# Kernel tuning notes

Hardware: AMD Instinct MI355X
Metric: run time of the kernel (lower is better)

## Reference

```python
import jax, jax.numpy as jnp
import numpy as np

H = 128   # hidden dim (all hidden_* params)
B = 256   # number of compound graphs in batch
NG = 4000  # number of compound groups (masked-out comp nodes)
NA = 10000  # number of anchors

LRELU = lambda x: jax.nn.leaky_relu(x, 0.1)
seg_sum = jax.ops.segment_sum


def seg_softmax(s, seg, n):
    # scatter_softmax over segments keyed by destination node
    m = jax.ops.segment_max(s, seg, num_segments=n)
    e = jnp.exp(s - m[seg])
    d = seg_sum(e, seg, num_segments=n)
    return e / d[seg]


def gru_cell(x, h, Wih, Whh, bih, bhh):
    # torch.nn.GRUCell semantics
    gi = x @ Wih.T + bih
    gh = h @ Whh.T + bhh
    ir, iz, inn = jnp.split(gi, 3, axis=-1)
    hr, hz, hn = jnp.split(gh, 3, axis=-1)
    r = jax.nn.sigmoid(ir + hr)
    z = jax.nn.sigmoid(iz + hz)
    n = jnp.tanh(inn + r * hn)
    return (1.0 - z) * n + z * h


def conv_stack(x, src, dst, Ws, bs, Wout, bout, n):
    # AtomConv/AnchorConv stack with dense-concat skip and output projection
    feats = [x]
    h = x
    for W, b in zip(Ws, bs):
        h = LRELU(seg_sum(h[src], dst, num_segments=n) @ W + b)
        feats.append(h)
    return LRELU(jnp.concatenate(feats, -1) @ Wout + bout)


def _forward(vert_x, site_x, masf_x, prot_edge_attr, prom_edge_attr,
             W_emb, b_emb,
             gwm_W_main, gwm_W_s2m, gwm_W_gate_main, gwm_b_gate_main,
             gwm_W_q, gwm_W_k, gwm_W_merge, gwm_W_gate_super, gwm_b_gate_super,
             gru_m_Wih, gru_m_Whh, gru_m_bih, gru_m_bhh,
             gru_s_Wih, gru_s_Whh, gru_s_bih, gru_s_bhh,
             W_site0, b_site0, W_site1, b_site1, W_site_out, b_site_out,
             W_masf0, b_masf0, W_masf1, b_masf1, W_masf_out, b_masf_out,
             W_anch0, b_anch0, W_anch1, b_anch1, W_anch_out, b_anch_out,
             W_dsite, b_dsite, W_dcomp, b_dcomp,
             vert_src, vert_dst, vert_batch, comp_src, comp_dst,
             site_src, site_dst, masf_src, masf_dst,
             prot_src, prot_dst, prom_src, prom_dst, anch_src, anch_dst,
             idx_ag_a, idx_ag_g, idx_aa_0, idx_aa_1, idx_gg_0, idx_gg_1):
    Nv = vert_x.shape[0]
    Ns = site_x.shape[0]
    Nm = masf_x.shape[0]
    # --- GraphConv_module: vertex embedding + super-node init ---
    vert = LRELU(vert_x @ W_emb + b_emb)
    supe = seg_sum(vert, vert_batch, num_segments=B)
    inv_sqrt_h = np.float32(1.0 / np.sqrt(H))
    # --- GWM iterations (shared GRU_main / GRU_super) ---
    for t in range(gwm_W_main.shape[0]):
        agg = seg_sum(vert[vert_src], vert_dst, num_segments=Nv)  # neighbor sum
        h_main = LRELU(agg @ gwm_W_main[t])
        trans = LRELU(supe @ gwm_W_s2m[t])[vert_batch]  # super -> main
        z = jax.nn.sigmoid(jnp.concatenate([h_main, trans], -1) @ gwm_W_gate_main[t] + gwm_b_gate_main[t])
        vert = gru_cell(z * h_main + (1.0 - z) * trans, vert,
                        gru_m_Wih, gru_m_Whh, gru_m_bih, gru_m_bhh)
        # main -> super attention (k_head = 1)
        q = (supe @ gwm_W_q[t])[vert_batch]
        k = vert @ gwm_W_k[t]
        score = jnp.sum(q * k, -1, keepdims=True) * inv_sqrt_h  # [Nv,1]
        attn = seg_softmax(score, vert_batch, B)
        pooled = seg_sum(attn * vert, vert_batch, num_segments=B)
        m_sup = LRELU(pooled @ gwm_W_merge[t])
        zs = jax.nn.sigmoid(jnp.concatenate([m_sup, supe], -1) @ gwm_W_gate_super[t] + gwm_b_gate_super[t])
        supe = gru_cell(zs * m_sup + (1.0 - zs) * supe, supe,
                        gru_s_Wih, gru_s_Whh, gru_s_bih, gru_s_bhh)
    # --- Group_module: uniform edge softmax (softmax of ones == 1/deg) ---
    w_g = seg_softmax(jnp.zeros((comp_src.shape[0], 1), vert.dtype), comp_dst, NG)
    group = seg_sum(w_g * vert[comp_src], comp_dst, num_segments=NG)  # [NG,H]
    # --- AtomConv_module / MasfConv_module ---
    site_out = conv_stack(site_x, site_src, site_dst, [W_site0, W_site1],
                          [b_site0, b_site1], W_site_out, b_site_out, Ns)
    masf_out = conv_stack(masf_x, masf_src, masf_dst, [W_masf0, W_masf1],
                          [b_masf0, b_masf1], W_masf_out, b_masf_out, Nm)
    # --- Anchor_module (UpwardConv with scatter_softmax(6 - dist) weights) ---
    # fill_anchor_graph's padded scatter + gather is fused into direct indexing
    w_p = seg_softmax(6.0 - prot_edge_attr, prot_dst, NA)
    anchor_atom = seg_sum(w_p * site_out[prot_src], prot_dst, num_segments=NA)
    w_m = seg_softmax(6.0 - prom_edge_attr, prom_dst, NA)
    anchor_masf = seg_sum(w_m * masf_out[prom_src], prom_dst, num_segments=NA)
    # --- AnchorAnchor_module (Affsrc == 'all': concat atom/masif anchor feats) ---
    anch = jnp.concatenate([anchor_atom, anchor_masf], -1)  # [NA,2H]
    anch_out = conv_stack(anch, anch_src, anch_dst, [W_anch0, W_anch1],
                          [b_anch0, b_anch1], W_anch_out, b_anch_out, NA)
    # --- Distance_pred_module ---
    pa = LRELU(anch_out @ W_dsite + b_dsite)
    pg = LRELU(group @ W_dcomp + b_dcomp)
    eps = np.float32(1e-6)  # torch.pairwise_distance eps
    pd = lambda a, b: jnp.sqrt(jnp.sum((a - b + eps) ** 2, -1, keepdims=True))
    ag = pd(pa[idx_ag_a], pg[idx_ag_g])
    aa = pd(pa[idx_aa_0], pa[idx_aa_1])
    gg = pd(pg[idx_gg_0], pg[idx_gg_1])
    return jnp.concatenate([ag, aa, gg], 0)  # [Pag+Paa+Pgg, 1]


def setup_inputs():
    key = jax.random.key(0)
    ks = iter(jax.random.split(key, 100))
    f32 = jnp.float32

    def nrm(shape, s=0.05):
        return jax.random.normal(next(ks), shape, f32) * s

    def ri(n, hi):
        return jax.random.randint(next(ks), (n,), 0, hi, dtype=jnp.int32)

    def zeros(*shape):
        return jnp.zeros(shape, f32)

    Nv, Ev, Ec = 20000, 80000, 40000
    Ns, Es = 80000, 320000
    Nm, Em = 80000, 320000
    Ep, Ea = 160000, 80000
    Pag, Paa, Pgg = 200000, 100000, 50000
    FV, Fs, Fm, D = 82, 256, 320, 2
    inp = {}
    inp["vert_x"] = nrm((Nv, FV), 1.0)
    inp["site_x"] = nrm((Ns, Fs), 1.0)
    inp["masf_x"] = nrm((Nm, Fm), 1.0)
    inp["prot_edge_attr"] = jax.random.uniform(next(ks), (Ep, 1), f32) * 6.0
    inp["prom_edge_attr"] = jax.random.uniform(next(ks), (Ep, 1), f32) * 6.0
    inp["vert_src"] = ri(Ev, Nv); inp["vert_dst"] = ri(Ev, Nv)
    inp["vert_batch"] = jnp.sort(ri(Nv, B))
    inp["comp_src"] = ri(Ec, Nv); inp["comp_dst"] = ri(Ec, NG)
    inp["site_src"] = ri(Es, Ns); inp["site_dst"] = ri(Es, Ns)
    inp["masf_src"] = ri(Em, Nm); inp["masf_dst"] = ri(Em, Nm)
    inp["prot_src"] = ri(Ep, Ns); inp["prot_dst"] = ri(Ep, NA)
    inp["prom_src"] = ri(Ep, Nm); inp["prom_dst"] = ri(Ep, NA)
    inp["anch_src"] = ri(Ea, NA); inp["anch_dst"] = ri(Ea, NA)
    inp["idx_ag_a"] = ri(Pag, NA); inp["idx_ag_g"] = ri(Pag, NG)
    inp["idx_aa_0"] = ri(Paa, NA); inp["idx_aa_1"] = ri(Paa, NA)
    inp["idx_gg_0"] = ri(Pgg, NG); inp["idx_gg_1"] = ri(Pgg, NG)
    inp["W_emb"] = nrm((FV, H)); inp["b_emb"] = zeros(H)
    inp["gwm_W_main"] = nrm((D, H, H)); inp["gwm_W_s2m"] = nrm((D, H, H))
    inp["gwm_W_gate_main"] = nrm((D, 2 * H, H)); inp["gwm_b_gate_main"] = zeros(D, H)
    inp["gwm_W_q"] = nrm((D, H, H)); inp["gwm_W_k"] = nrm((D, H, H))
    inp["gwm_W_merge"] = nrm((D, H, H))
    inp["gwm_W_gate_super"] = nrm((D, 2 * H, H)); inp["gwm_b_gate_super"] = zeros(D, H)
    for p in ["m", "s"]:
        inp["gru_%s_Wih" % p] = nrm((3 * H, H)); inp["gru_%s_Whh" % p] = nrm((3 * H, H))
        inp["gru_%s_bih" % p] = zeros(3 * H); inp["gru_%s_bhh" % p] = zeros(3 * H)
    inp["W_site0"] = nrm((Fs, H)); inp["b_site0"] = zeros(H)
    inp["W_site1"] = nrm((H, H)); inp["b_site1"] = zeros(H)
    inp["W_site_out"] = nrm((Fs + 2 * H, H)); inp["b_site_out"] = zeros(H)
    inp["W_masf0"] = nrm((Fm, H)); inp["b_masf0"] = zeros(H)
    inp["W_masf1"] = nrm((H, H)); inp["b_masf1"] = zeros(H)
    inp["W_masf_out"] = nrm((Fm + 2 * H, H)); inp["b_masf_out"] = zeros(H)
    inp["W_anch0"] = nrm((2 * H, H)); inp["b_anch0"] = zeros(H)
    inp["W_anch1"] = nrm((H, H)); inp["b_anch1"] = zeros(H)
    inp["W_anch_out"] = nrm((4 * H, H)); inp["b_anch_out"] = zeros(H)
    inp["W_dsite"] = nrm((H, H)); inp["b_dsite"] = zeros(H)
    inp["W_dcomp"] = nrm((H, H)); inp["b_dcomp"] = zeros(H)
    return inp


def reference(vert_x, site_x, masf_x, prot_edge_attr, prom_edge_attr,
              W_emb, b_emb,
              gwm_W_main, gwm_W_s2m, gwm_W_gate_main, gwm_b_gate_main,
              gwm_W_q, gwm_W_k, gwm_W_merge, gwm_W_gate_super, gwm_b_gate_super,
              gru_m_Wih, gru_m_Whh, gru_m_bih, gru_m_bhh,
              gru_s_Wih, gru_s_Whh, gru_s_bih, gru_s_bhh,
              W_site0, b_site0, W_site1, b_site1, W_site_out, b_site_out,
              W_masf0, b_masf0, W_masf1, b_masf1, W_masf_out, b_masf_out,
              W_anch0, b_anch0, W_anch1, b_anch1, W_anch_out, b_anch_out,
              W_dsite, b_dsite, W_dcomp, b_dcomp,
              vert_src, vert_dst, vert_batch, comp_src, comp_dst,
              site_src, site_dst, masf_src, masf_dst,
              prot_src, prot_dst, prom_src, prom_dst, anch_src, anch_dst,
              idx_ag_a, idx_ag_g, idx_aa_0, idx_aa_1, idx_gg_0, idx_gg_1):
    return _forward(vert_x, site_x, masf_x, prot_edge_attr, prom_edge_attr,
                    W_emb, b_emb,
                    gwm_W_main, gwm_W_s2m, gwm_W_gate_main, gwm_b_gate_main,
                    gwm_W_q, gwm_W_k, gwm_W_merge, gwm_W_gate_super, gwm_b_gate_super,
                    gru_m_Wih, gru_m_Whh, gru_m_bih, gru_m_bhh,
                    gru_s_Wih, gru_s_Whh, gru_s_bih, gru_s_bhh,
                    W_site0, b_site0, W_site1, b_site1, W_site_out, b_site_out,
                    W_masf0, b_masf0, W_masf1, b_masf1, W_masf_out, b_masf_out,
                    W_anch0, b_anch0, W_anch1, b_anch1, W_anch_out, b_anch_out,
                    W_dsite, b_dsite, W_dcomp, b_dcomp,
                    vert_src, vert_dst, vert_batch, comp_src, comp_dst,
                    site_src, site_dst, masf_src, masf_dst,
                    prot_src, prot_dst, prom_src, prom_dst, anch_src, anch_dst,
                    idx_ag_a, idx_ag_g, idx_aa_0, idx_aa_1, idx_gg_0, idx_gg_1)
```

## Files before the change

### kernel.cpp

```cpp
#include <hip/hip_runtime.h>
#include <math.h>

#define HD 128

typedef __bf16 bf16x8 __attribute__((ext_vector_type(8)));
typedef unsigned short u16x8 __attribute__((ext_vector_type(8)));
typedef float f32x4 __attribute__((ext_vector_type(4)));

__device__ __forceinline__ unsigned short f2bf(float f) {
    unsigned u = __float_as_uint(f);
    unsigned r = u + 0x7FFFu + ((u >> 16) & 1u);
    return (unsigned short)(r >> 16);
}

#define MAXW 32
struct WDesc { const float* src; unsigned short* dst; int K, N, Kpad, tr; };
struct WBatch { WDesc d[MAXW]; };

__global__ void convert_weights(WBatch wb)
{
    WDesc d = wb.d[blockIdx.y];
    long total = (long)d.N * d.Kpad;
    long i = (long)blockIdx.x * 256 + threadIdx.x;
    if (i >= total) return;
    int n = (int)(i / d.Kpad), k = (int)(i % d.Kpad);
    float v = 0.f;
    if (k < d.K) v = d.tr ? d.src[(size_t)k * d.N + n] : d.src[(size_t)n * d.K + k];
    d.dst[i] = f2bf(v);
}

__global__ __launch_bounds__(256)
void gemm_mfma(const float* __restrict__ A0, const float* __restrict__ A1,
               const float* __restrict__ A2, int K0, int K1, int K2,
               int lda0, int lda1, int lda2,
               const unsigned short* __restrict__ WT, int Kpad,
               const float* __restrict__ bias, float* __restrict__ C,
               int M, int N, int act,
               const float* __restrict__ G1, const float* __restrict__ G2)
{
    __shared__ __align__(16) unsigned short sA[2][64][40];
    __shared__ __align__(16) unsigned short sW[2][128][40];

    const int tid = threadIdx.x;
    const int lane = tid & 63, w = tid >> 6;
    const int mBase = blockIdx.x * 64;
    const int nBase = blockIdx.y * 128;
    const int Ktot = K0 + K1 + K2;
    const int colb = w * 32;
    const int c16 = lane & 15, g = lane >> 4;

    f32x4 acc[4][2];
#pragma unroll
    for (int i = 0; i < 4; ++i)
#pragma unroll
        for (int j = 0; j < 2; ++j) acc[i][j] = (f32x4){0.f, 0.f, 0.f, 0.f};

    const int kTiles = (Ktot + 31) / 32;

    auto loadTile = [&](int kt, float f[8], u16x8& h0, u16x8& h1) {
        const int k0g = kt * 32;
        const float* Ab; int lda, kloc, segK;
        if (k0g < K0)           { Ab = A0; lda = lda0; kloc = k0g;           segK = K0; }
        else if (k0g < K0 + K1) { Ab = A1; lda = lda1; kloc = k0g - K0;      segK = K1; }
        else                    { Ab = A2; lda = lda2; kloc = k0g - K0 - K1; segK = K2; }
        int row = tid >> 2, kq = (tid & 3) * 8;
        int gr = mBase + row;
        if (gr < M && ((lda & 3) == 0) && (kloc + kq + 8 <= segK)) {
            const float* ap = Ab + (size_t)gr * lda + kloc + kq;
            float4 v0 = *(const float4*)ap, v1 = *(const float4*)(ap + 4);
            f[0] = v0.x; f[1] = v0.y; f[2] = v0.z; f[3] = v0.w;
            f[4] = v1.x; f[5] = v1.y; f[6] = v1.z; f[7] = v1.w;
        } else {
#pragma unroll
            for (int i = 0; i < 8; ++i) {
                int kk = kloc + kq + i;
                f[i] = (gr < M && kk < segK) ? Ab[(size_t)gr * lda + kk] : 0.f;
            }
        }
        int col = tid >> 1, kh = (tid & 1) * 16;
        const unsigned short* wp = WT + (size_t)(nBase + col) * Kpad + k0g + kh;
        h0 = *(const u16x8*)wp;
        h1 = *(const u16x8*)(wp + 8);
    };
    auto stageWrite = [&](int buf, const float f[8], u16x8 h0, u16x8 h1) {
        int row = tid >> 2, kq = (tid & 3) * 8;
        u16x8 h;
#pragma unroll
        for (int i = 0; i < 8; ++i) h[i] = f2bf(f[i]);
        *(u16x8*)&sA[buf][row][kq] = h;
        int col = tid >> 1, kh = (tid & 1) * 16;
        *(u16x8*)&sW[buf][col][kh] = h0;
        *(u16x8*)&sW[buf][col][kh + 8] = h1;
    };
    auto compute = [&](int buf) {
        bf16x8 bfr0 = __builtin_bit_cast(bf16x8, *(const u16x8*)&sW[buf][colb + c16][g * 8]);
        bf16x8 bfr1 = __builtin_bit_cast(bf16x8, *(const u16x8*)&sW[buf][colb + 16 + c16][g * 8]);
#pragma unroll
        for (int rf = 0; rf < 4; ++rf) {
            bf16x8 af = __builtin_bit_cast(bf16x8, *(const u16x8*)&sA[buf][rf * 16 + c16][g * 8]);
            acc[rf][0] = __builtin_amdgcn_mfma_f32_16x16x32_bf16(af, bfr0, acc[rf][0], 0, 0, 0);
            acc[rf][1] = __builtin_amdgcn_mfma_f32_16x16x32_bf16(af, bfr1, acc[rf][1], 0, 0, 0);
        }
    };

    float fN[8]; u16x8 hN0, hN1;
    {
        float fC[8]; u16x8 hC0, hC1;
        loadTile(0, fC, hC0, hC1);
        stageWrite(0, fC, hC0, hC1);
        if (kTiles > 1) loadTile(1, fN, hN0, hN1);
    }
    asm volatile("s_waitcnt lgkmcnt(0)" ::: "memory");
    __builtin_amdgcn_s_barrier();

    int cur = 0;
#pragma unroll 2
    for (int kt = 0; kt < kTiles; ++kt) {
        float fP[8]; u16x8 hP0, hP1;
        const bool pf = (kt + 2 < kTiles);
        if (pf) loadTile(kt + 2, fP, hP0, hP1);
        compute(cur);
        if (kt + 1 < kTiles) stageWrite(cur ^ 1, fN, hN0, hN1);
        asm volatile("s_waitcnt lgkmcnt(0)" ::: "memory");
        __builtin_amdgcn_s_barrier();
        if (pf) {
#pragma unroll
            for (int i = 0; i < 8; ++i) fN[i] = fP[i];
            hN0 = hP0; hN1 = hP1;
        }
        cur ^= 1;
    }

#pragma unroll
    for (int cf = 0; cf < 2; ++cf) {
        int col = nBase + colb + cf * 16 + c16;
        float bb = bias ? bias[col] : 0.f;
#pragma unroll
        for (int rf = 0; rf < 4; ++rf) {
            int r0 = mBase + rf * 16 + g * 4;
#pragma unroll
            for (int r = 0; r < 4; ++r) {
                int gr = r0 + r;
                if (gr >= M) continue;
                size_t o = (size_t)gr * N + col;
                float v = acc[rf][cf][r] + bb;
                if (act == 1) v = v > 0.f ? v : 0.1f * v;
                else if (act == 2) v = 1.f / (1.f + expf(-v));
                else if (act == 3) {
                    float z = 1.f / (1.f + expf(-v));
                    v = z * G1[o] + (1.f - z) * G2[o];
                }
                C[o] = v;
            }
        }
    }
}

__global__ void hist_k(int* __restrict__ cnt, const int* __restrict__ dst, int E)
{
    int i = blockIdx.x * 256 + threadIdx.x;
    if (i < E) atomicAdd(&cnt[dst[i]], 1);
}

#define SCB 4096

__global__ __launch_bounds__(256)
void scan_sums(const int* __restrict__ cnt, int n, int* __restrict__ bsum)
{
    __shared__ int red[256];
    int t = threadIdx.x;
    int base = blockIdx.x * SCB + t * 16;
    int s = 0;
#pragma unroll
    for (int i = 0; i < 16; ++i) { int idx = base + i; if (idx < n) s += cnt[idx]; }
    red[t] = s; __syncthreads();
    for (int st = 128; st > 0; st >>= 1) {
        if (t < st) red[t] += red[t + st];
        __syncthreads();
    }
    if (t == 0) bsum[blockIdx.x] = red[0];
}

__global__ void scan_bsum(int* __restrict__ bsum, int nb)
{
    if (threadIdx.x == 0) {
// ... 8 lines not shown
{
    __shared__ int a0[256], a1[256];
    int t = threadIdx.x;
    int base = blockIdx.x * SCB + t * 16;
    int v[16]; int s = 0;
#pragma unroll
    for (int i = 0; i < 16; ++i) { int idx = base + i; v[i] = (idx < n) ? cnt[idx] : 0; s += v[i]; }
    a0[t] = s; __syncthreads();
    int* cur = a0; int* nxt = a1;
    for (int st = 1; st < 256; st <<= 1) {
        int val = cur[t] + ((t >= st) ? cur[t - st] : 0);
        nxt[t] = val; __syncthreads();
        int* tmp = cur; cur = nxt; nxt = tmp;
    }
    int run = bsum[blockIdx.x] + (t > 0 ? cur[t - 1] : 0);
#pragma unroll
    for (int i = 0; i < 16; ++i) {
        int idx = base + i;
        if (idx < n) {
            rp[idx] = run; run += v[i];
            if (idx == n - 1) rp[n] = run;
        }
    }
}

__global__ void fill_k(int* __restrict__ eidx, int* __restrict__ cursor,
                       const int* __restrict__ dst, int E)
{
    int i = blockIdx.x * 256 + threadIdx.x;
    if (i < E) eidx[atomicAdd(&cursor[dst[i]], 1)] = i;
}

__global__ __launch_bounds__(256)
void seg_gather(float* __restrict__ out, const float* __restrict__ X,
                const int* __restrict__ rowptr, const int* __restrict__ eidx,
                const int* __restrict__ src, const float* __restrict__ wattr,
                const float* __restrict__ bias, int n, int ostride, int ooff,
                int act, int mode)
{
    int d = blockIdx.x * 4 + (threadIdx.x >> 6);
    if (d >= n) return;
    int lane = threadIdx.x & 63;
    int lo = rowptr[d], hi = rowptr[d + 1];
    float w0 = 1.f, mx = 0.f, iden = 0.f;
    if (mode == 2) w0 = (hi > lo) ? 1.f / (float)(hi - lo) : 0.f;
    if (mode == 3) {
        float mxl = -1e30f;
        for (int base = lo; base < hi; base += 64) {
            int i = base + lane;
            if (i < hi) mxl = fmaxf(mxl, 6.f - wattr[eidx[i]]);
        }
#pragma unroll
        for (int o = 32; o; o >>= 1) mxl = fmaxf(mxl, __shfl_xor(mxl, o));
        mx = mxl;
        float dl = 0.f;
        for (int base = lo; base < hi; base += 64) {
            int i = base + lane;
            if (i < hi) dl += expf(6.f - wattr[eidx[i]] - mx);
        }
#pragma unroll
        for (int o = 32; o; o >>= 1) dl += __shfl_xor(dl, o);
        iden = 1.f / dl;
    }

    float ax = 0.f, ay = 0.f;
    int i = lo;
    for (; i + 4 <= hi; i += 4) {
        int e0 = eidx[i], e1 = eidx[i + 1], e2 = eidx[i + 2], e3 = eidx[i + 3];
        int s0 = src ? src[e0] : e0, s1 = src ? src[e1] : e1;
        int s2 = src ? src[e2] : e2, s3 = src ? src[e3] : e3;
        float w0v, w1v, w2v, w3v;
        if (mode == 0) { w0v = w1v = w2v = w3v = 1.f; }
        else if (mode == 1) { w0v = wattr[e0]; w1v = wattr[e1]; w2v = wattr[e2]; w3v = wattr[e3]; }
        else if (mode == 2) { w0v = w1v = w2v = w3v = w0; }
        else {
            w0v = expf(6.f - wattr[e0] - mx) * iden;
            w1v = expf(6.f - wattr[e1] - mx) * iden;
            w2v = expf(6.f - wattr[e2] - mx) * iden;
            w3v = expf(6.f - wattr[e3] - mx) * iden;
        }
        float2 v0 = *(const float2*)(X + (size_t)s0 * HD + 2 * lane);
        float2 v1 = *(const float2*)(X + (size_t)s1 * HD + 2 * lane);
        float2 v2 = *(const float2*)(X + (size_t)s2 * HD + 2 * lane);
        float2 v3 = *(const float2*)(X + (size_t)s3 * HD + 2 * lane);
        ax += w0v * v0.x + w1v * v1.x + w2v * v2.x + w3v * v3.x;
        ay += w0v * v0.y + w1v * v1.y + w2v * v2.y + w3v * v3.y;
    }
    for (; i < hi; ++i) {
        int e = eidx[i];
        int s = src ? src[e] : e;
        float w;
        if (mode == 0) w = 1.f;
        else if (mode == 1) w = wattr[e];
        else if (mode == 2) w = w0;
        else w = expf(6.f - wattr[e] - mx) * iden;
        float2 v = *(const float2*)(X + (size_t)s * HD + 2 * lane);
        ax += w * v.x; ay += w * v.y;
    }
    if (bias) { float2 b = *(const float2*)(bias + 2 * lane); ax += b.x; ay += b.y; }
    if (act == 1) { ax = ax > 0.f ? ax : 0.1f * ax; ay = ay > 0.f ? ay : 0.1f * ay; }
    *(float2*)(out + (size_t)d * ostride + ooff + 2 * lane) = make_float2(ax, ay);
}

__global__ __launch_bounds__(256)
void seg_softmax_csr(float* __restrict__ sc, const int* __restrict__ rowptr,
                     const int* __restrict__ eidx, int n)
{
    int d = blockIdx.x * 4 + (threadIdx.x >> 6);
    if (d >= n) return;
    int lane = threadIdx.x & 63;
    int lo = rowptr[d], hi = rowptr[d + 1];
    float mxl = -1e30f;
    for (int i = lo + lane; i < hi; i += 64) mxl = fmaxf(mxl, sc[eidx[i]]);
#pragma unroll
    for (int o = 32; o; o >>= 1) mxl = fmaxf(mxl, __shfl_xor(mxl, o));
    float dl = 0.f;
    for (int i = lo + lane; i < hi; i += 64) dl += expf(sc[eidx[i]] - mxl);
#pragma unroll
    for (int o = 32; o; o >>= 1) dl += __shfl_xor(dl, o);
    float iden = 1.f / dl;
    for (int i = lo + lane; i < hi; i += 64) {
        int v = eidx[i];
        sc[v] = expf(sc[v] - mxl) * iden;
    }
}

__global__ void gather128(float* __restrict__ out, const float* __restrict__ in,
                          const int* __restrict__ idx, int n)
{
    long i = (long)blockIdx.x * 256 + threadIdx.x;
    if (i >= (long)n * HD) return;
    int r = (int)(i >> 7), f = (int)(i & 127);
    out[i] = in[(size_t)idx[r] * HD + f];
}
// ... 22 lines not shown
#pragma unroll
    for (int i = 0; i < 32; ++i) {
        float4 x = a[i], y = q[i];
        acc += x.x * y.x + x.y * y.y + x.z * y.z + x.w * y.w;
    }
    sc[v] = acc * 0.08838834764831843f;
}

__global__ void pdist_k(float* __restrict__ out, const float* __restrict__ A,
                        const float* __restrict__ Bm, const int* __restrict__ ia,
                        const int* __restrict__ ib, int P)
{
    int p = blockIdx.x * 256 + threadIdx.x;
    if (p >= P) return;
    const float4* a = (const float4*)(A + (size_t)ia[p] * HD);
    const float4* b = (const float4*)(Bm + (size_t)ib[p] * HD);
    float acc = 0.f;
#pragma unroll
    for (int i = 0; i < 32; ++i) {
        float4 x = a[i], y = b[i];
        float d0 = x.x - y.x + 1e-6f, d1 = x.y - y.y + 1e-6f;
        float d2 = x.z - y.z + 1e-6f, d3 = x.w - y.w + 1e-6f;
        acc += d0 * d0 + d1 * d1 + d2 * d2 + d3 * d3;
    }
    out[p] = sqrtf(acc);
}


static inline unsigned gupd(size_t n) { return (unsigned)((n + 255) / 256); }
static inline unsigned gup4(size_t n) { return (unsigned)((n + 3) / 4); }

struct WArena { unsigned short* p; int Kpad; };

static void gemm3s(hipStream_t st, const float* A0, int K0, const float* A1, int K1,
                   const float* A2, int K2, WArena wa, const float* bias,
                   float* C, int M, int N, int act,
                   const float* G1 = nullptr, const float* G2 = nullptr)
{
    dim3 g((M + 63) / 64, N / 128);
    hipLaunchKernelGGL(gemm_mfma, g, dim3(256), 0, st, A0, A1, A2, K0, K1, K2,
                       K0, K1, K2, wa.p, wa.Kpad, bias, C, M, N, act, G1, G2);
}
static void gemm1(hipStream_t st, const float* A, int K, WArena wa, const float* bias,
                  float* C, int M, int N, int act)
{ gemm3s(st, A, K, nullptr, 0, nullptr, 0, wa, bias, C, M, N, act); }
static void gemm2g(hipStream_t st, const float* A0, int K0, const float* A1, int K1,
                   WArena wa, const float* bias, float* C, int M, int N, int act,
                   const float* G1 = nullptr, const float* G2 = nullptr)
{ gemm3s(st, A0, K0, A1, K1, nullptr, 0, wa, bias, C, M, N, act, G1, G2); }

extern "C" void kernel_launch(void* const* d_in, const int* in_sizes, int n_in,
                              void* d_out, int out_size, void* d_ws, size_t ws_size,
                              hipStream_t stream)
{
    (void)n_in; (void)out_size;
    const float* vert_x  = (const float*)d_in[0];
    const float* site_x  = (const float*)d_in[1];
    const float* masf_x  = (const float*)d_in[2];
    const float* prot_ea = (const float*)d_in[3];
    const float* prom_ea = (const float*)d_in[4];
    const int* vert_src = (const int*)d_in[5];
    const int* vert_dst = (const int*)d_in[6];
    const int* vbatch   = (const int*)d_in[7];
    const int* comp_src = (const int*)d_in[8];
    const int* comp_dst = (const int*)d_in[9];
    const int* site_src = (const int*)d_in[10];
    const int* site_dst = (const int*)d_in[11];
    const int* masf_src = (const int*)d_in[12];
    const int* masf_dst = (const int*)d_in[13];
    const int* prot_src = (const int*)d_in[14];
    const int* prot_dst = (const int*)d_in[15];
    const int* prom_src = (const int*)d_in[16];
    const int* prom_dst = (const int*)d_in[17];
    const int* anch_src = (const int*)d_in[18];
    const int* anch_dst = (const int*)d_in[19];
    const int* ag_a = (const int*)d_in[20];
    const int* ag_g = (const int*)d_in[21];
    const int* aa0  = (const int*)d_in[22];
    const int* aa1  = (const int*)d_in[23];
    const int* gg0  = (const int*)d_in[24];
    const int* gg1  = (const int*)d_in[25];
    const float* W_emb = (const float*)d_in[26];
// ... 30 lines not shown
    const float* W_a0 = (const float*)d_in[57];
    const float* b_a0 = (const float*)d_in[58];
    const float* W_a1 = (const float*)d_in[59];
    const float* b_a1 = (const float*)d_in[60];
    const float* W_ao = (const float*)d_in[61];
    const float* b_ao = (const float*)d_in[62];
    const float* W_ds = (const float*)d_in[63];
    const float* b_ds = (const float*)d_in[64];
    const float* W_dc = (const float*)d_in[65];
    const float* b_dc = (const float*)d_in[66];

    const int B = 256, NG = 4000, NA = 10000, Ns = 80000, Nm = 80000;
    const int Nv = in_sizes[7];
    const int FV = in_sizes[0] / Nv;
    const int Fs = in_sizes[1] / Ns;
    const int Fm = in_sizes[2] / Nm;
    const int Ev = in_sizes[5], Ec = in_sizes[8], Es = in_sizes[10], Em = in_sizes[12];
    const int Ep = in_sizes[14], Ea = in_sizes[18];
    const int Pag = in_sizes[20], Paa = in_sizes[22], Pgg = in_sizes[24];
    const int D = in_sizes[28] / (HD * HD);

    float* ws = (float*)d_ws;
    size_t off = 0;
    auto take = [&](size_t n) { size_t o = off; off += n; return o; };
    float* vert  = ws + take((size_t)Nv * HD);
    float* supe  = ws + take((size_t)B * HD);
    float* qsup  = ws + take((size_t)B * HD);
    float* pool  = ws + take((size_t)B * HD);
    float* msup  = ws + take((size_t)B * HD);
    float* zsup  = ws + take((size_t)B * HD);
    float* gis   = ws + take((size_t)B * 3 * HD);
    float* ghs   = ws + take((size_t)B * 3 * HD);
    float* tsml  = ws + take((size_t)B * HD);
    float* grp   = ws + take((size_t)NG * HD);
    float* site_o = ws + take((size_t)Ns * HD);
    float* masf_o = ws + take((size_t)Nm * HD);
    float* anch  = ws + take((size_t)NA * 2 * HD);
    float* ah1   = ws + take((size_t)NA * HD);
    float* ah2   = ws + take((size_t)NA * HD);
    float* axw   = ws + take((size_t)NA * HD);
    float* aout  = ws + take((size_t)NA * HD);
    float* pa    = ws + take((size_t)NA * HD);
    float* pg    = ws + take((size_t)NG * HD);
    float* score = ws + take((size_t)Nv);
    const size_t NvH = (size_t)Nv * HD, NsH = (size_t)Ns * HD;
    float* T = ws + take(3 * NsH);

    const int nN[8] = {Nv, NG, Ns, Nm, NA, NA, NA, B};
    const int nE[8] = {Ev, Ec, Es, Em, Ep, Ep, Ea, Nv};
    const int* dsts[8] = {vert_dst, comp_dst, site_dst, masf_dst,
                          prot_dst, prom_dst, anch_dst, vbatch};
    int baseN[9], baseE[9];
    baseN[0] = 0; baseE[0] = 0;
    for (int g = 0; g < 8; ++g) { baseN[g + 1] = baseN[g] + nN[g]; baseE[g + 1] = baseE[g] + nE[g]; }
    const int totN = baseN[8], totE = baseE[8];

    int* ib = (int*)(ws + off);
    size_t ioff = 0;
    auto taki = [&](size_t n) { size_t o = ioff; ioff += n; return o; };
    int* cnt_all = ib + taki((size_t)totN);
    int* rp_all  = ib + taki((size_t)totN + 1);
    int* cur_all = ib + taki((size_t)totN);
    int* ei_all  = ib + taki((size_t)totE);
    int* bsum    = ib + taki((size_t)((totN + SCB - 1) / SCB) + 1);
    ioff = (ioff + 7) & ~(size_t)7;

    unsigned short* warena = (unsigned short*)(ib + ioff);
    size_t woff = 0;
    WBatch wb; int nW = 0; long maxWTot = 0;
    auto reg = [&](const float* src, int K, int N, int tr) {
        int Kpad = (K + 31) & ~31;
        unsigned short* dst = warena + woff;
        woff += (size_t)N * Kpad;
        long tot = (long)N * Kpad; if (tot > maxWTot) maxWTot = tot;
// ... 28 lines not shown
    WArena wa_ao = reg(W_ao, 4 * HD, HD, 1);
    WArena wa_ds = reg(W_ds, HD, HD, 1);
    WArena wa_dc = reg(W_dc, HD, HD, 1);

    if (ws_size < off * sizeof(float) + ioff * sizeof(int) + woff * sizeof(unsigned short))
        return;

    {
        dim3 g((unsigned)((maxWTot + 255) / 256), nW);
        hipLaunchKernelGGL(convert_weights, g, dim3(256), 0, stream, wb);
    }

    hipMemsetAsync(cnt_all, 0, (size_t)totN * sizeof(int), stream);
    for (int g = 0; g < 8; ++g)
        hist_k<<<gupd((size_t)nE[g]), 256, 0, stream>>>(cnt_all + baseN[g], dsts[g], nE[g]);
    const int nScanBlocks = (totN + SCB - 1) / SCB;
    scan_sums<<<nScanBlocks, 256, 0, stream>>>(cnt_all, totN, bsum);
    scan_bsum<<<1, 64, 0, stream>>>(bsum, nScanBlocks);
    scan_write<<<nScanBlocks, 256, 0, stream>>>(cnt_all, totN, bsum, rp_all);
    hipMemcpyAsync(cur_all, rp_all, (size_t)totN * sizeof(int), hipMemcpyDeviceToDevice, stream);
    for (int g = 0; g < 8; ++g)
        fill_k<<<gupd((size_t)nE[g]), 256, 0, stream>>>(ei_all, cur_all + baseN[g], dsts[g], nE[g]);

    const int* rp_v = rp_all + baseN[0];
    const int* rp_c = rp_all + baseN[1];
    const int* rp_s = rp_all + baseN[2];
    const int* rp_m = rp_all + baseN[3];
    const int* rp_p = rp_all + baseN[4];
    const int* rp_q = rp_all + baseN[5];
    const int* rp_a = rp_all + baseN[6];
    const int* rp_b = rp_all + baseN[7];
    const int* ei = ei_all;

    gemm1(stream, vert_x, FV, wa_emb, b_emb, vert, Nv, HD, 1);
    seg_gather<<<gup4(B), 256, 0, stream>>>(supe, vert, rp_b, ei, nullptr, nullptr,
                                            nullptr, B, HD, 0, 0, 0);

    float* Ta = T;            float* Tb = T + NvH;     float* Tc = T + 2 * NvH;
    float* Td = T + 3 * NvH;  float* Te = T + 4 * NvH; float* Tf = T + 7 * NvH;
    for (int t = 0; t < D; ++t) {
        const float* bgm = gb_gm + (size_t)t * HD;
        const float* bgs = gb_gs + (size_t)t * HD;

        gemm1(stream, vert, HD, wa_main[t], nullptr, Ta, Nv, HD, 0);
        seg_gather<<<gup4((size_t)Nv), 256, 0, stream>>>(Tb, Ta, rp_v, ei, vert_src,
                                                         nullptr, nullptr, Nv, HD, 0, 1, 0);
        gemm1(stream, supe, HD, wa_s2m[t], nullptr, tsml, B, HD, 1);
        gather128<<<gupd(NvH), 256, 0, stream>>>(Tc, tsml, vbatch, Nv);
        gemm2g(stream, Tb, HD, Tc, HD, wa_gm[t], bgm, Td, Nv, HD, 3, Tb, Tc);
        gemm1(stream, Td, HD, wa_mih, gm_bih, Te, Nv, 3 * HD, 0);
        gemm1(stream, vert, HD, wa_mhh, gm_bhh, Tf, Nv, 3 * HD, 0);
        gru_gate<<<gupd(NvH), 256, 0, stream>>>(vert, Te, Tf, Nv);
        gemm1(stream, vert, HD, wa_k[t], nullptr, Ta, Nv, HD, 0);
        gemm1(stream, supe, HD, wa_q[t], nullptr, qsup, B, HD, 0);
        dot_score<<<gupd((size_t)Nv), 256, 0, stream>>>(score, Ta, qsup, vbatch, Nv);
        seg_softmax_csr<<<gup4(B), 256, 0, stream>>>(score, rp_b, ei, B);
        seg_gather<<<gup4(B), 256, 0, stream>>>(pool, vert, rp_b, ei, nullptr, score,
                                                nullptr, B, HD, 0, 0, 1);
        gemm1(stream, pool, HD, wa_mrg[t], nullptr, msup, B, HD, 1);
        gemm2g(stream, msup, HD, supe, HD, wa_gs[t], bgs, zsup, B, HD, 3, msup, supe);
        gemm1(stream, zsup, HD, wa_sih, gs_bih, gis, B, 3 * HD, 0);
        gemm1(stream, supe, HD, wa_shh, gs_bhh, ghs, B, 3 * HD, 0);
        gru_gate<<<gupd((size_t)B * HD), 256, 0, stream>>>(supe, gis, ghs, B);
    }

    seg_gather<<<gup4((size_t)NG), 256, 0, stream>>>(grp, vert, rp_c, ei, comp_src,
                                                     nullptr, nullptr, NG, HD, 0, 0, 2);

    float* T1 = T; float* T2 = T + NsH; float* T3 = T + 2 * NsH;
    gemm1(stream, site_x, Fs, wa_s0, nullptr, T1, Ns, HD, 0);
    seg_gather<<<gup4((size_t)Ns), 256, 0, stream>>>(T2, T1, rp_s, ei, site_src,
                                                     nullptr, b_s0, Ns, HD, 0, 1, 0);
    gemm1(stream, T2, HD, wa_s1, nullptr, T1, Ns, HD, 0);
    seg_gather<<<gup4((size_t)Ns), 256, 0, stream>>>(T3, T1, rp_s, ei, site_src,
                                                     nullptr, b_s1, Ns, HD, 0, 1, 0);
    gemm3s(stream, site_x, Fs, T2, HD, T3, HD, wa_so, b_so, site_o, Ns, HD, 1);

    gemm1(stream, masf_x, Fm, wa_m0, nullptr, T1, Nm, HD, 0);
    seg_gather<<<gup4((size_t)Nm), 256, 0, stream>>>(T2, T1, rp_m, ei, masf_src,
                                                     nullptr, b_m0, Nm, HD, 0, 1, 0);
    gemm1(stream, T2, HD, wa_m1, nullptr, T1, Nm, HD, 0);
    seg_gather<<<gup4((size_t)Nm), 256, 0, stream>>>(T3, T1, rp_m, ei, masf_src,
                                                     nullptr, b_m1, Nm, HD, 0, 1, 0);
    gemm3s(stream, masf_x, Fm, T2, HD, T3, HD, wa_mo, b_mo, masf_o, Nm, HD, 1);

    seg_gather<<<gup4((size_t)NA), 256, 0, stream>>>(anch, site_o, rp_p, ei, prot_src,
                                                     prot_ea, nullptr, NA, 2 * HD, 0, 0, 3);
    seg_gather<<<gup4((size_t)NA), 256, 0, stream>>>(anch, masf_o, rp_q, ei, prom_src,
                                                     prom_ea, nullptr, NA, 2 * HD, HD, 0, 3);

    gemm1(stream, anch, 2 * HD, wa_a0, nullptr, axw, NA, HD, 0);
    seg_gather<<<gup4((size_t)NA), 256, 0, stream>>>(ah1, axw, rp_a, ei, anch_src,
                                                     nullptr, b_a0, NA, HD, 0, 1, 0);
    gemm1(stream, ah1, HD, wa_a1, nullptr, axw, NA, HD, 0);
    seg_gather<<<gup4((size_t)NA), 256, 0, stream>>>(ah2, axw, rp_a, ei, anch_src,
                                                     nullptr, b_a1, NA, HD, 0, 1, 0);
    gemm3s(stream, anch, 2 * HD, ah1, HD, ah2, HD, wa_ao, b_ao, aout, NA, HD, 1);

    gemm1(stream, aout, HD, wa_ds, b_ds, pa, NA, HD, 1);
    gemm1(stream, grp, HD, wa_dc, b_dc, pg, NG, HD, 1);
    float* outp = (float*)d_out;
    pdist_k<<<gupd((size_t)Pag), 256, 0, stream>>>(outp, pa, pg, ag_a, ag_g, Pag);
    pdist_k<<<gupd((size_t)Paa), 256, 0, stream>>>(outp + Pag, pa, pa, aa0, aa1, Paa);
    pdist_k<<<gupd((size_t)Pgg), 256, 0, stream>>>(outp + Pag + Paa, pg, pg, gg0, gg1, Pgg);
}
```

Measured before the change: 1.330 ms.

## Store site/masf/anchor intermediates in bf16 to halve gather and GEMM traffic

Adds bf16 input and output modes to the MFMA GEMM and the segment-gather kernel, then keeps the site, masf, anchor and compound-group intermediate activations in bf16 instead of fp32. This roughly halves the bytes moved by the irregular gathers and the GEMM A-operand loads, and skips the fp32-to-bf16 conversion that was already done inside the GEMM. In exchange, accumulated values are rounded to bf16 between layers, which adds numerical error, and every call carries per-call dtype flags and extra branches.

New measurement: 1.411 ms. 6.1% more time.

```diff
diff --git a/kernel.cpp b/kernel.cpp
--- a/kernel.cpp
+++ b/kernel.cpp
@@ -11,6 +11,15 @@
     unsigned u = __float_as_uint(f);
     unsigned r = u + 0x7FFFu + ((u >> 16) & 1u);
     return (unsigned short)(r >> 16);
+}
+
+__device__ __forceinline__ float2 ldrow2(const void* X, size_t off, int xbf) {
+    if (xbf) {
+        unsigned u = *(const unsigned*)((const unsigned short*)X + off);
+        return make_float2(__uint_as_float((u & 0xffffu) << 16),
+                           __uint_as_float((u >> 16) << 16));
+    }
+    return *(const float2*)((const float*)X + off);
 }
 
 #define MAXW 32
@@ -30,12 +39,12 @@
 }
 
 __global__ __launch_bounds__(256)
-void gemm_mfma(const float* __restrict__ A0, const float* __restrict__ A1,
-               const float* __restrict__ A2, int K0, int K1, int K2,
-               int lda0, int lda1, int lda2,
+void gemm_mfma(const void* __restrict__ A0, const void* __restrict__ A1,
+               const void* __restrict__ A2, int K0, int K1, int K2,
+               int lda0, int lda1, int lda2, int dt0, int dt1, int dt2,
                const unsigned short* __restrict__ WT, int Kpad,
-               const float* __restrict__ bias, float* __restrict__ C,
-               int M, int N, int act,
+               const float* __restrict__ bias, void* __restrict__ Cv,
+               int M, int N, int act, int obf,
                const float* __restrict__ G1, const float* __restrict__ G2)
 {
     __shared__ __align__(16) unsigned short sA[2][64][40];
@@ -57,24 +66,34 @@
 
     const int kTiles = (Ktot + 31) / 32;
 
-    auto loadTile = [&](int kt, float f[8], u16x8& h0, u16x8& h1) {
+    auto loadTile = [&](int kt, float f[8], u16x8& ha, int& isbf, u16x8& h0, u16x8& h1) {
         const int k0g = kt * 32;
-        const float* Ab; int lda, kloc, segK;
-        if (k0g < K0)           { Ab = A0; lda = lda0; kloc = k0g;           segK = K0; }
-        else if (k0g < K0 + K1) { Ab = A1; lda = lda1; kloc = k0g - K0;      segK = K1; }
-        else                    { Ab = A2; lda = lda2; kloc = k0g - K0 - K1; segK = K2; }
+        const void* Ab; int lda, kloc, segK;
+        if (k0g < K0)           { Ab = A0; lda = lda0; kloc = k0g;           segK = K0; isbf = dt0; }
+        else if (k0g < K0 + K1) { Ab = A1; lda = lda1; kloc = k0g - K0;      segK = K1; isbf = dt1; }
+        else                    { Ab = A2; lda = lda2; kloc = k0g - K0 - K1; segK = K2; isbf = dt2; }
         int row = tid >> 2, kq = (tid & 3) * 8;
         int gr = mBase + row;
-        if (gr < M && ((lda & 3) == 0) && (kloc + kq + 8 <= segK)) {
-            const float* ap = Ab + (size_t)gr * lda + kloc + kq;
-            float4 v0 = *(const float4*)ap, v1 = *(const float4*)(ap + 4);
-            f[0] = v0.x; f[1] = v0.y; f[2] = v0.z; f[3] = v0.w;
-            f[4] = v1.x; f[5] = v1.y; f[6] = v1.z; f[7] = v1.w;
+        if (isbf) {
+            u16x8 z;
+#pragma unroll
+            for (int i = 0; i < 8; ++i) z[i] = 0;
+            ha = (gr < M && kloc + kq + 8 <= segK)
+                 ? *(const u16x8*)((const unsigned short*)Ab + (size_t)gr * lda + kloc + kq)
+                 : z;
         } else {
-#pragma unroll
-            for (int i = 0; i < 8; ++i) {
-                int kk = kloc + kq + i;
-                f[i] = (gr < M && kk < segK) ? Ab[(size_t)gr * lda + kk] : 0.f;
+            const float* Af = (const float*)Ab;
+            if (gr < M && ((lda & 3) == 0) && (kloc + kq + 8 <= segK)) {
+                const float* ap = Af + (size_t)gr * lda + kloc + kq;
+                float4 v0 = *(const float4*)ap, v1 = *(const float4*)(ap + 4);
+                f[0] = v0.x; f[1] = v0.y; f[2] = v0.z; f[3] = v0.w;
+                f[4] = v1.x; f[5] = v1.y; f[6] = v1.z; f[7] = v1.w;
+            } else {
+#pragma unroll
+                for (int i = 0; i < 8; ++i) {
+                    int kk = kloc + kq + i;
+                    f[i] = (gr < M && kk < segK) ? Af[(size_t)gr * lda + kk] : 0.f;
+                }
             }
         }
         int col = tid >> 1, kh = (tid & 1) * 16;
@@ -82,11 +101,14 @@
         h0 = *(const u16x8*)wp;
         h1 = *(const u16x8*)(wp + 8);
     };
-    auto stageWrite = [&](int buf, const float f[8], u16x8 h0, u16x8 h1) {
+    auto stageWrite = [&](int buf, int isbf, const float f[8], u16x8 ha, u16x8 h0, u16x8 h1) {
         int row = tid >> 2, kq = (tid & 3) * 8;
         u16x8 h;
-#pragma unroll
-        for (int i = 0; i < 8; ++i) h[i] = f2bf(f[i]);
+        if (isbf) h = ha;
+        else {
+#pragma unroll
+            for (int i = 0; i < 8; ++i) h[i] = f2bf(f[i]);
+        }
         *(u16x8*)&sA[buf][row][kq] = h;
         int col = tid >> 1, kh = (tid & 1) * 16;
         *(u16x8*)&sW[buf][col][kh] = h0;
@@ -103,12 +125,12 @@
         }
     };
 
-    float fN[8]; u16x8 hN0, hN1;
+    float fN[8]; u16x8 haN, hN0, hN1; int bfN = 0;
     {
-        float fC[8]; u16x8 hC0, hC1;
-        loadTile(0, fC, hC0, hC1);
-        stageWrite(0, fC, hC0, hC1);
-        if (kTiles > 1) loadTile(1, fN, hN0, hN1);
+        float fC[8]; u16x8 haC, hC0, hC1; int bfC;
+        loadTile(0, fC, haC, bfC, hC0, hC1);
+        stageWrite(0, bfC, fC, haC, hC0, hC1);
+        if (kTiles > 1) loadTile(1, fN, haN, bfN, hN0, hN1);
     }
     asm volatile("s_waitcnt lgkmcnt(0)" ::: "memory");
     __builtin_amdgcn_s_barrier();
@@ -116,17 +138,17 @@
     int cur = 0;
 #pragma unroll 2
     for (int kt = 0; kt < kTiles; ++kt) {
-        float fP[8]; u16x8 hP0, hP1;
+        float fP[8]; u16x8 haP, hP0, hP1; int bfP = 0;
         const bool pf = (kt + 2 < kTiles);
-        if (pf) loadTile(kt + 2, fP, hP0, hP1);
+        if (pf) loadTile(kt + 2, fP, haP, bfP, hP0, hP1);
         compute(cur);
-        if (kt + 1 < kTiles) stageWrite(cur ^ 1, fN, hN0, hN1);
+        if (kt + 1 < kTiles) stageWrite(cur ^ 1, bfN, fN, haN, hN0, hN1);
         asm volatile("s_waitcnt lgkmcnt(0)" ::: "memory");
         __builtin_amdgcn_s_barrier();
         if (pf) {
 #pragma unroll
             for (int i = 0; i < 8; ++i) fN[i] = fP[i];
-            hN0 = hP0; hN1 = hP1;
+            haN = haP; hN0 = hP0; hN1 = hP1; bfN = bfP;
         }
         cur ^= 1;
     }
@@ -150,7 +172,8 @@
                     float z = 1.f / (1.f + expf(-v));
                     v = z * G1[o] + (1.f - z) * G2[o];
                 }
-                C[o] = v;
+                if (obf) ((unsigned short*)Cv)[o] = f2bf(v);
+                else     ((float*)Cv)[o] = v;
             }
         }
     }
@@ -225,11 +248,11 @@
 }
 
 __global__ __launch_bounds__(256)
-void seg_gather(float* __restrict__ out, const float* __restrict__ X,
+void seg_gather(void* __restrict__ out, const void* __restrict__ X,
                 const int* __restrict__ rowptr, const int* __restrict__ eidx,
                 const int* __restrict__ src, const float* __restrict__ wattr,
                 const float* __restrict__ bias, int n, int ostride, int ooff,
-                int act, int mode)
+                int act, int mode, int xbf, int obf)
 {
     int d = blockIdx.x * 4 + (threadIdx.x >> 6);
     if (d >= n) return;
@@ -272,10 +295,10 @@
             w2v = expf(6.f - wattr[e2] - mx) * iden;
             w3v = expf(6.f - wattr[e3] - mx) * iden;
         }
-        float2 v0 = *(const float2*)(X + (size_t)s0 * HD + 2 * lane);
-        float2 v1 = *(const float2*)(X + (size_t)s1 * HD + 2 * lane);
-        float2 v2 = *(const float2*)(X + (size_t)s2 * HD + 2 * lane);
-        float2 v3 = *(const float2*)(X + (size_t)s3 * HD + 2 * lane);
+        float2 v0 = ldrow2(X, (size_t)s0 * HD + 2 * lane, xbf);
+        float2 v1 = ldrow2(X, (size_t)s1 * HD + 2 * lane, xbf);
+        float2 v2 = ldrow2(X, (size_t)s2 * HD + 2 * lane, xbf);
+        float2 v3 = ldrow2(X, (size_t)s3 * HD + 2 * lane, xbf);
         ax += w0v * v0.x + w1v * v1.x + w2v * v2.x + w3v * v3.x;
         ay += w0v * v0.y + w1v * v1.y + w2v * v2.y + w3v * v3.y;
     }
@@ -287,12 +310,18 @@
         else if (mode == 1) w = wattr[e];
         else if (mode == 2) w = w0;
         else w = expf(6.f - wattr[e] - mx) * iden;
-        float2 v = *(const float2*)(X + (size_t)s * HD + 2 * lane);
+        float2 v = ldrow2(X, (size_t)s * HD + 2 * lane, xbf);
         ax += w * v.x; ay += w * v.y;
     }
     if (bias) { float2 b = *(const float2*)(bias + 2 * lane); ax += b.x; ay += b.y; }
     if (act == 1) { ax = ax > 0.f ? ax : 0.1f * ax; ay = ay > 0.f ? ay : 0.1f * ay; }
-    *(float2*)(out + (size_t)d * ostride + ooff + 2 * lane) = make_float2(ax, ay);
+    size_t o = (size_t)d * ostride + ooff + 2 * lane;
+    if (obf) {
+        unsigned u = (unsigned)f2bf(ax) | ((unsigned)f2bf(ay) << 16);
+        *(unsigned*)((unsigned short*)out + o) = u;
+    } else {
+        *(float2*)((float*)out + o) = make_float2(ax, ay);
+    }
 }
 
 __global__ __launch_bounds__(256)
@@ -381,22 +410,21 @@
 
 struct WArena { unsigned short* p; int Kpad; };
 
-static void gemm3s(hipStream_t st, const float* A0, int K0, const float* A1, int K1,
-                   const float* A2, int K2, WArena wa, const float* bias,
-                   float* C, int M, int N, int act,
-                   const float* G1 = nullptr, const float* G2 = nullptr)
+static void gemmX(hipStream_t st, const void* A0, int K0, int dt0,
+                  const void* A1, int K1, int dt1,
+                  const void* A2, int K2, int dt2,
+                  WArena wa, const float* bias, void* C, int M, int N,
+                  int act, int obf,
+                  const float* G1 = nullptr, const float* G2 = nullptr)
 {
     dim3 g((M + 63) / 64, N / 128);
     hipLaunchKernelGGL(gemm_mfma, g, dim3(256), 0, st, A0, A1, A2, K0, K1, K2,
-                       K0, K1, K2, wa.p, wa.Kpad, bias, C, M, N, act, G1, G2);
-}
-static void gemm1(hipStream_t st, const float* A, int K, WArena wa, const float* bias,
-                  float* C, int M, int N, int act)
-{ gemm3s(st, A, K, nullptr, 0, nullptr, 0, wa, bias, C, M, N, act); }
-static void gemm2g(hipStream_t st, const float* A0, int K0, const float* A1, int K1,
-                   WArena wa, const float* bias, float* C, int M, int N, int act,
-                   const float* G1 = nullptr, const float* G2 = nullptr)
-{ gemm3s(st, A0, K0, A1, K1, nullptr, 0, wa, bias, C, M, N, act, G1, G2); }
+                       K0, K1, K2, dt0, dt1, dt2, wa.p, wa.Kpad, bias, C, M, N,
+                       act, obf, G1, G2);
+}
+static void gemm1(hipStream_t st, const void* A, int K, int dt, WArena wa,
+                  const float* bias, void* C, int M, int N, int act, int obf)
+{ gemmX(st, A, K, dt, nullptr, 0, 0, nullptr, 0, 0, wa, bias, C, M, N, act, obf); }
 
 extern "C" void kernel_launch(void* const* d_in, const int* in_sizes, int n_in,
                               void* d_out, int out_size, void* d_ws, size_t ws_size,
@@ -493,14 +521,14 @@
     float* gis   = ws + take((size_t)B * 3 * HD);
     float* ghs   = ws + take((size_t)B * 3 * HD);
     float* tsml  = ws + take((size_t)B * HD);
-    float* grp   = ws + take((size_t)NG * HD);
-    float* site_o = ws + take((size_t)Ns * HD);
-    float* masf_o = ws + take((size_t)Nm * HD);
-    float* anch  = ws + take((size_t)NA * 2 * HD);
-    float* ah1   = ws + take((size_t)NA * HD);
-    float* ah2   = ws + take((size_t)NA * HD);
-    float* axw   = ws + take((size_t)NA * HD);
-    float* aout  = ws + take((size_t)NA * HD);
+    unsigned short* grp_h    = (unsigned short*)(ws + take((size_t)NG * HD));
+    unsigned short* site_o_h = (unsigned short*)(ws + take((size_t)Ns * HD));
+    unsigned short* masf_o_h = (unsigned short*)(ws + take((size_t)Nm * HD));
+    unsigned short* anch_h   = (unsigned short*)(ws + take((size_t)NA * 2 * HD));
+    unsigned short* ah1_h    = (unsigned short*)(ws + take((size_t)NA * HD));
+    unsigned short* ah2_h    = (unsigned short*)(ws + take((size_t)NA * HD));
+    unsigned short* axw_h    = (unsigned short*)(ws + take((size_t)NA * HD));
+    unsigned short* aout_h   = (unsigned short*)(ws + take((size_t)NA * HD));
     float* pa    = ws + take((size_t)NA * HD);
     float* pg    = ws + take((size_t)NG * HD);
     float* score = ws + take((size_t)Nv);
@@ -595,9 +623,9 @@
     const int* rp_b = rp_all + baseN[7];
     const int* ei = ei_all;
 
-    gemm1(stream, vert_x, FV, wa_emb, b_emb, vert, Nv, HD, 1);
+    gemm1(stream, vert_x, FV, 0, wa_emb, b_emb, vert, Nv, HD, 1, 0);
     seg_gather<<<gup4(B), 256, 0, stream>>>(supe, vert, rp_b, ei, nullptr, nullptr,
-                                            nullptr, B, HD, 0, 0, 0);
+                                            nullptr, B, HD, 0, 0, 0, 0, 0);
 
     float* Ta = T;            float* Tb = T + NvH;     float* Tc = T + 2 * NvH;
     float* Td = T + 3 * NvH;  float* Te = T + 4 * NvH; float* Tf = T + 7 * NvH;
@@ -605,63 +633,65 @@
         const float* bgm = gb_gm + (size_t)t * HD;
         const float* bgs = gb_gs + (size_t)t * HD;
 
-        gemm1(stream, vert, HD, wa_main[t], nullptr, Ta, Nv, HD, 0);
+        gemm1(stream, vert, HD, 0, wa_main[t], nullptr, Ta, Nv, HD, 0, 0);
         seg_gather<<<gup4((size_t)Nv), 256, 0, stream>>>(Tb, Ta, rp_v, ei, vert_src,
-                                                         nullptr, nullptr, Nv, HD, 0, 1, 0);
-        gemm1(stream, supe, HD, wa_s2m[t], nullptr, tsml, B, HD, 1);
+                                                         nullptr, nullptr, Nv, HD, 0, 1, 0, 0, 0);
+        gemm1(stream, supe, HD, 0, wa_s2m[t], nullptr, tsml, B, HD, 1, 0);
         gather128<<<gupd(NvH), 256, 0, stream>>>(Tc, tsml, vbatch, Nv);
-        gemm2g(stream, Tb, HD, Tc, HD, wa_gm[t], bgm, Td, Nv, HD, 3, Tb, Tc);
-        gemm1(stream, Td, HD, wa_mih, gm_bih, Te, Nv, 3 * HD, 0);
-        gemm1(stream, vert, HD, wa_mhh, gm_bhh, Tf, Nv, 3 * HD, 0);
+        gemmX(stream, Tb, HD, 0, Tc, HD, 0, nullptr, 0, 0, wa_gm[t], bgm, Td, Nv, HD, 3, 0, Tb, Tc);
+        gemm1(stream, Td, HD, 0, wa_mih, gm_bih, Te, Nv, 3 * HD, 0, 0);
+        gemm1(stream, vert, HD, 0, wa_mhh, gm_bhh, Tf, Nv, 3 * HD, 0, 0);
         gru_gate<<<gupd(NvH), 256, 0, stream>>>(vert, Te, Tf, Nv);
-        gemm1(stream, vert, HD, wa_k[t], nullptr, Ta, Nv, HD, 0);
-        gemm1(stream, supe, HD, wa_q[t], nullptr, qsup, B, HD, 0);
+        gemm1(stream, vert, HD, 0, wa_k[t], nullptr, Ta, Nv, HD, 0, 0);
+        gemm1(stream, supe, HD, 0, wa_q[t], nullptr, qsup, B, HD, 0, 0);
         dot_score<<<gupd((size_t)Nv), 256, 0, stream>>>(score, Ta, qsup, vbatch, Nv);
         seg_softmax_csr<<<gup4(B), 256, 0, stream>>>(score, rp_b, ei, B);
         seg_gather<<<gup4(B), 256, 0, stream>>>(pool, vert, rp_b, ei, nullptr, score,
-                                                nullptr, B, HD, 0, 0, 1);
-        gemm1(stream, pool, HD, wa_mrg[t], nullptr, msup, B, HD, 1);
-        gemm2g(stream, msup, HD, supe, HD, wa_gs[t], bgs, zsup, B, HD, 3, msup, supe);
-        gemm1(stream, zsup, HD, wa_sih, gs_bih, gis, B, 3 * HD, 0);
-        gemm1(stream, supe, HD, wa_shh, gs_bhh, ghs, B, 3 * HD, 0);
+                                                nullptr, B, HD, 0, 0, 1, 0, 0);
+        gemm1(stream, pool, HD, 0, wa_mrg[t], nullptr, msup, B, HD, 1, 0);
+        gemmX(stream, msup, HD, 0, supe, HD, 0, nullptr, 0, 0, wa_gs[t], bgs, zsup, B, HD, 3, 0, msup, supe);
+        gemm1(stream, zsup, HD, 0, wa_sih, gs_bih, gis, B, 3 * HD, 0, 0);
+        gemm1(stream, supe, HD, 0, wa_shh, gs_bhh, ghs, B, 3 * HD, 0, 0);
         gru_gate<<<gupd((size_t)B * HD), 256, 0, stream>>>(supe, gis, ghs, B);
     }
 
-    seg_gather<<<gup4((size_t)NG), 256, 0, stream>>>(grp, vert, rp_c, ei, comp_src,
-                                                     nullptr, nullptr, NG, HD, 0, 0, 2);
-
-    float* T1 = T; float* T2 = T + NsH; float* T3 = T + 2 * NsH;
-    gemm1(stream, site_x, Fs, wa_s0, nullptr, T1, Ns, HD, 0);
-    seg_gather<<<gup4((size_t)Ns), 256, 0, stream>>>(T2, T1, rp_s, ei, site_src,
-                                                     nullptr, b_s0, Ns, HD, 0, 1, 0);
-    gemm1(stream, T2, HD, wa_s1, nullptr, T1, Ns, HD, 0);
-    seg_gather<<<gup4((size_t)Ns), 256, 0, stream>>>(T3, T1, rp_s, ei, site_src,
-                                                     nullptr, b_s1, Ns, HD, 0, 1, 0);
-    gemm3s(stream, site_x, Fs, T2, HD, T3, HD, wa_so, b_so, site_o, Ns, HD, 1);
-
-    gemm1(stream, masf_x, Fm, wa_m0, nullptr, T1, Nm, HD, 0);
-    seg_gather<<<gup4((size_t)Nm), 256, 0, stream>>>(T2, T1, rp_m, ei, masf_src,
-                                                     nullptr, b_m0, Nm, HD, 0, 1, 0);
-    gemm1(stream, T2, HD, wa_m1, nullptr, T1, Nm, HD, 0);
-    seg_gather<<<gup4((size_t)Nm), 256, 0, stream>>>(T3, T1, rp_m, ei, masf_src,
-                                                     nullptr, b_m1, Nm, HD, 0, 1, 0);
-    gemm3s(stream, masf_x, Fm, T2, HD, T3, HD, wa_mo, b_mo, masf_o, Nm, HD, 1);
-
-    seg_gather<<<gup4((size_t)NA), 256, 0, stream>>>(anch, site_o, rp_p, ei, prot_src,
-                                                     prot_ea, nullptr, NA, 2 * HD, 0, 0, 3);
-    seg_gather<<<gup4((size_t)NA), 256, 0, stream>>>(anch, masf_o, rp_q, ei, prom_src,
-                                                     prom_ea, nullptr, NA, 2 * HD, HD, 0, 3);
-
-    gemm1(stream, anch, 2 * HD, wa_a0, nullptr, axw, NA, HD, 0);
-    seg_gather<<<gup4((size_t)NA), 256, 0, stream>>>(ah1, axw, rp_a, ei, anch_src,
-                                                     nullptr, b_a0, NA, HD, 0, 1, 0);
-    gemm1(stream, ah1, HD, wa_a1, nullptr, axw, NA, HD, 0);
-    seg_gather<<<gup4((size_t)NA), 256, 0, stream>>>(ah2, axw, rp_a, ei, anch_src,
-                                                     nullptr, b_a1, NA, HD, 0, 1, 0);
-    gemm3s(stream, anch, 2 * HD, ah1, HD, ah2, HD, wa_ao, b_ao, aout, NA, HD, 1);
-
-    gemm1(stream, aout, HD, wa_ds, b_ds, pa, NA, HD, 1);
-    gemm1(stream, grp, HD, wa_dc, b_dc, pg, NG, HD, 1);
+    seg_gather<<<gup4((size_t)NG), 256, 0, stream>>>(grp_h, vert, rp_c, ei, comp_src,
+                                                     nullptr, nullptr, NG, HD, 0, 0, 2, 0, 1);
+
+    unsigned short* T1h = (unsigned short*)T;
+    unsigned short* T2h = (unsigned short*)(T + NsH);
+    unsigned short* T3h = (unsigned short*)(T + 2 * NsH);
+    gemm1(stream, site_x, Fs, 0, wa_s0, nullptr, T1h, Ns, HD, 0, 1);
+    seg_gather<<<gup4((size_t)Ns), 256, 0, stream>>>(T2h, T1h, rp_s, ei, site_src,
+                                                     nullptr, b_s0, Ns, HD, 0, 1, 0, 1, 1);
+    gemm1(stream, T2h, HD, 1, wa_s1, nullptr, T1h, Ns, HD, 0, 1);
+    seg_gather<<<gup4((size_t)Ns), 256, 0, stream>>>(T3h, T1h, rp_s, ei, site_src,
+                                                     nullptr, b_s1, Ns, HD, 0, 1, 0, 1, 1);
+    gemmX(stream, site_x, Fs, 0, T2h, HD, 1, T3h, HD, 1, wa_so, b_so, site_o_h, Ns, HD, 1, 1);
+
+    gemm1(stream, masf_x, Fm, 0, wa_m0, nullptr, T1h, Nm, HD, 0, 1);
+    seg_gather<<<gup4((size_t)Nm), 256, 0, stream>>>(T2h, T1h, rp_m, ei, masf_src,
+                                                     nullptr, b_m0, Nm, HD, 0, 1, 0, 1, 1);
+    gemm1(stream, T2h, HD, 1, wa_m1, nullptr, T1h, Nm, HD, 0, 1);
+    seg_gather<<<gup4((size_t)Nm), 256, 0, stream>>>(T3h, T1h, rp_m, ei, masf_src,
+                                                     nullptr, b_m1, Nm, HD, 0, 1, 0, 1, 1);
+    gemmX(stream, masf_x, Fm, 0, T2h, HD, 1, T3h, HD, 1, wa_mo, b_mo, masf_o_h, Nm, HD, 1, 1);
+
+    seg_gather<<<gup4((size_t)NA), 256, 0, stream>>>(anch_h, site_o_h, rp_p, ei, prot_src,
+                                                     prot_ea, nullptr, NA, 2 * HD, 0, 0, 3, 1, 1);
+    seg_gather<<<gup4((size_t)NA), 256, 0, stream>>>(anch_h, masf_o_h, rp_q, ei, prom_src,
+                                                     prom_ea, nullptr, NA, 2 * HD, HD, 0, 3, 1, 1);
+
+    gemm1(stream, anch_h, 2 * HD, 1, wa_a0, nullptr, axw_h, NA, HD, 0, 1);
+    seg_gather<<<gup4((size_t)NA), 256, 0, stream>>>(ah1_h, axw_h, rp_a, ei, anch_src,
+                                                     nullptr, b_a0, NA, HD, 0, 1, 0, 1, 1);
+    gemm1(stream, ah1_h, HD, 1, wa_a1, nullptr, axw_h, NA, HD, 0, 1);
+    seg_gather<<<gup4((size_t)NA), 256, 0, stream>>>(ah2_h, axw_h, rp_a, ei, anch_src,
+                                                     nullptr, b_a1, NA, HD, 0, 1, 0, 1, 1);
+    gemmX(stream, anch_h, 2 * HD, 1, ah1_h, HD, 1, ah2_h, HD, 1, wa_ao, b_ao, aout_h, NA, HD, 1, 1);
+
+    gemm1(stream, aout_h, HD, 1, wa_ds, b_ds, pa, NA, HD, 1, 0);
+    gemm1(stream, grp_h, HD, 1, wa_dc, b_dc, pg, NG, HD, 1, 0);
     float* outp = (float*)d_out;
     pdist_k<<<gupd((size_t)Pag), 256, 0, stream>>>(outp, pa, pg, ag_a, ag_g, Pag);
     pdist_k<<<gupd((size_t)Paa), 256, 0, stream>>>(outp + Pag, pa, pa, aa0, aa1, Paa);
```
